# Kernel optimization log

Measured on AMD Instinct MI355X. Metric: run time of the kernel, lower is better.

## Reference

```python
import math
import jax, jax.numpy as jnp
import numpy as np

B, D, C = 2048, 512, 50000
M = math.pi / 6.0
S = 15.0
COS_M, SIN_M = math.cos(M), math.sin(M)
TH = math.cos(math.pi - M)
MM = math.sin(math.pi - M) * M
EPS = 1e-12


def setup_inputs() -> dict:
    key = jax.random.key(0)
    k1, k2, k3 = jax.random.split(key, 3)
    x = jax.random.normal(k1, (B, D), dtype=jnp.float32)
    label = jax.random.randint(k2, (B,), 0, C, dtype=jnp.int64)
    # xavier_normal_ on [C, D]: std = sqrt(2 / (C + D))
    std = math.sqrt(2.0 / (C + D))
    weight = jax.random.normal(k3, (C, D), dtype=jnp.float32) * std
    return {"x": x, "label": label, "weight": weight}


def reference(x, label, weight):
    # L2-normalize rows (F.normalize with eps clamp)
    xn = x / jnp.maximum(jnp.linalg.norm(x, axis=1, keepdims=True), EPS)
    wn = weight / jnp.maximum(jnp.linalg.norm(weight, axis=1, keepdims=True), EPS)
    cosine = xn @ wn.T  # [B, C]

    rows = jnp.arange(cosine.shape[0])
    cos_t = cosine[rows, label]  # target-class cosines [B]
    sin_t = jnp.sqrt(jnp.clip(1.0 - cos_t * cos_t, 0.0, 1.0))
    phi_t = cos_t * COS_M - sin_t * SIN_M
    # easy_margin = False branch
    phi_t = jnp.where(cos_t - TH > 0, phi_t, cos_t - MM)

    # one_hot * phi + (1 - one_hot) * cosine, then scale
    output = S * cosine.at[rows, label].set(phi_t)  # [B, C]

    logp = jax.nn.log_softmax(output, axis=1)
    loss = -jnp.mean(logp[rows, label])
    return output, loss
```

## Files before the change

kernel.cpp:

```cpp
#include <hip/hip_runtime.h>

#define B_ 2048
#define D_ 512
#define C_ 50000
#define NTILEN 391
#define NPART (NTILEN * 2)

static constexpr float S_SCALE = 15.0f;
static constexpr float COS_M_ = 0.86602540378443864676f;
static constexpr float SIN_M_ = 0.5f;
static constexpr float TH_    = -0.86602540378443864676f;
static constexpr float MM_    = 0.26179938779914943654f;

typedef unsigned short u16;
typedef __attribute__((ext_vector_type(4))) float f32x4;
typedef __attribute__((ext_vector_type(8))) short s16x8;

__device__ __forceinline__ u16 f2bf(float f) {
  unsigned u = __float_as_uint(f);
  u += 0x7fffu + ((u >> 16) & 1u);
  return (u16)(u >> 16);
}

__device__ __forceinline__ void load_lds16(const void* g, void* l) {
  __builtin_amdgcn_global_load_lds((const __attribute__((address_space(1))) void*)g,
                                   (__attribute__((address_space(3))) void*)l,
                                   16, 0, 0);
}

__global__ void rownorm_kernel(const float* __restrict__ src, u16* __restrict__ dst,
                               float* __restrict__ loss_zero) {
  const int row = blockIdx.x;
  const int tid = threadIdx.x;
  const float4* s = (const float4*)(src + (size_t)row * D_);
  float4 v = s[tid];
  float ss = v.x * v.x + v.y * v.y + v.z * v.z + v.w * v.w;
#pragma unroll
  for (int mask = 1; mask < 64; mask <<= 1) ss += __shfl_xor(ss, mask);
  __shared__ float red[2];
  if ((tid & 63) == 0) red[tid >> 6] = ss;
  __syncthreads();
  float total = red[0] + red[1];
  float inv = 1.0f / fmaxf(sqrtf(total), 1e-12f);
  ushort4 o;
  o.x = f2bf(v.x * inv); o.y = f2bf(v.y * inv);
  o.z = f2bf(v.z * inv); o.w = f2bf(v.w * inv);
  ((ushort4*)(dst + (size_t)row * D_))[tid] = o;
  if (loss_zero && row == 0 && tid == 0) *loss_zero = 0.0f;
}

__global__ __launch_bounds__(256) void aam_gemm_kernel(
    const u16* __restrict__ xn, const u16* __restrict__ wn,
    const int* __restrict__ label, float* __restrict__ out,
    float* __restrict__ partial, float* __restrict__ target) {
  __shared__ u16 sA[128 * 64];
  __shared__ u16 sB[128 * 64];
  __shared__ int sLbl[128];

  const int tid = threadIdx.x;
  const int m0 = blockIdx.x * 128;
  const int n0 = blockIdx.y * 128;
  const int wave = tid >> 6;
  const int lane = tid & 63;
  const int wm = wave >> 1;
  const int wn_ = wave & 1;

  if (tid < 128) sLbl[tid] = label[m0 + tid];

  f32x4 acc[4][4];
#pragma unroll
  for (int i = 0; i < 4; ++i)
#pragma unroll
    for (int j = 0; j < 4; ++j) {
      f32x4 z = {0.0f, 0.0f, 0.0f, 0.0f};
      acc[i][j] = z;
    }

  for (int kt = 0; kt < D_ / 64; ++kt) {
    const int k0 = kt * 64;
    __syncthreads();
#pragma unroll
    for (int j = 0; j < 4; ++j) {
      const int L = j * 256 + tid;
      const int m = L >> 3;
      const int cs = L & 7;
      const int kc = cs ^ (m & 7);
      load_lds16(xn + (size_t)(m0 + m) * D_ + k0 + kc * 8, &sA[L * 8]);
    }
#pragma unroll
    for (int j = 0; j < 4; ++j) {
      const int L = j * 256 + tid;
      const int m = L >> 3;
      const int cs = L & 7;
      const int kc = cs ^ (m & 7);
      int wr = n0 + m;
      if (wr >= C_) wr = 0;
      load_lds16(wn + (size_t)wr * D_ + k0 + kc * 8, &sB[L * 8]);
    }
    __syncthreads();

#pragma unroll
    for (int kk = 0; kk < 2; ++kk) {
      const int chunk = kk * 4 + (lane >> 4);
      s16x8 af[4], bf[4];
#pragma unroll
      for (int mf = 0; mf < 4; ++mf) {
        const int r = wm * 64 + mf * 16 + (lane & 15);
        const int cs = chunk ^ (r & 7);
        af[mf] = *(const s16x8*)&sA[r * 64 + cs * 8];
      }
#pragma unroll
      for (int nf = 0; nf < 4; ++nf) {
        const int r = wn_ * 64 + nf * 16 + (lane & 15);
        const int cs = chunk ^ (r & 7);
        bf[nf] = *(const s16x8*)&sB[r * 64 + cs * 8];
      }
#pragma unroll
      for (int mf = 0; mf < 4; ++mf)
#pragma unroll
        for (int nf = 0; nf < 4; ++nf)
          acc[mf][nf] = __builtin_amdgcn_mfma_f32_16x16x32_bf16(af[mf], bf[nf],
                                                                acc[mf][nf], 0, 0, 0);
    }
  }

  const int colbase = n0 + wn_ * 64 + (lane & 15);
#pragma unroll
  for (int mf = 0; mf < 4; ++mf) {
#pragma unroll
    for (int reg = 0; reg < 4; ++reg) {
      const int row_l = wm * 64 + mf * 16 + ((lane >> 4) << 2) + reg;
      const int row_g = m0 + row_l;
      const int lbl = sLbl[row_l];
      float v[4];
      float vmax = -INFINITY;
#pragma unroll
      for (int nf = 0; nf < 4; ++nf) {
        const int col = colbase + nf * 16;
        float cv = acc[mf][nf][reg];
        float val = S_SCALE * cv;
        if (col == lbl) {
          float st = sqrtf(fminf(fmaxf(1.0f - cv * cv, 0.0f), 1.0f));
          float phi = cv * COS_M_ - st * SIN_M_;
          float pv = (cv - TH_ > 0.0f) ? phi : (cv - MM_);
          val = S_SCALE * pv;
          target[row_g] = val;
        }
        if (col < C_) {
          out[(size_t)row_g * C_ + col] = val;
          v[nf] = val;
          vmax = fmaxf(vmax, val);
        } else {
          v[nf] = -INFINITY;
        }
      }
#pragma unroll
      for (int mask = 1; mask < 16; mask <<= 1)
        vmax = fmaxf(vmax, __shfl_xor(vmax, mask));
      float sev = 0.0f;
#pragma unroll
      for (int nf = 0; nf < 4; ++nf)
        if (v[nf] != -INFINITY) sev += __expf(v[nf] - vmax);
#pragma unroll
      for (int mask = 1; mask < 16; mask <<= 1) sev += __shfl_xor(sev, mask);
      if ((lane & 15) == 0) {
        float* p = partial + ((size_t)row_g * NPART + (blockIdx.y * 2 + wn_)) * 2;
        p[0] = vmax;
        p[1] = sev;
      }
    }
  }
}

__global__ __launch_bounds__(256) void loss_kernel(const float* __restrict__ partial,
                                                   const float* __restrict__ target,
                                                   float* __restrict__ loss) {
  const int lane = threadIdx.x & 63;
  const int row = blockIdx.x * 4 + (threadIdx.x >> 6);
  float m = -INFINITY, l = 0.0f;
  const float2* p = (const float2*)partial + (size_t)row * NPART;
  for (int i = lane; i < NPART; i += 64) {
    float2 q = p[i];
    if (q.x > m) {
      l = l * __expf(m - q.x) + q.y;
      m = q.x;
    } else if (q.x != -INFINITY) {
      l += q.y * __expf(q.x - m);
    }
  }
#pragma unroll
  for (int mask = 1; mask < 64; mask <<= 1) {
    float m2 = __shfl_xor(m, mask);
    float l2 = __shfl_xor(l, mask);
    if (m2 > m) {
      l = l * __expf(m - m2) + l2;
      m = m2;
    } else if (m2 != -INFINITY) {
      l += l2 * __expf(m2 - m);
    }
  }
  __shared__ float sred[4];
  if (lane == 0) sred[threadIdx.x >> 6] = (m + logf(l)) - target[row];
  __syncthreads();
  if (threadIdx.x == 0)
    atomicAdd(loss, (sred[0] + sred[1] + sred[2] + sred[3]) * (1.0f / 2048.0f));
}

extern "C" void kernel_launch(void* const* d_in, const int* in_sizes, int n_in,
                              void* d_out, int out_size, void* d_ws, size_t ws_size,
                              hipStream_t stream) {
  const float* x = (const float*)d_in[0];
  const int* label = (const int*)d_in[1];
  const float* w = (const float*)d_in[2];
  float* out = (float*)d_out;
  float* loss = out + (size_t)B_ * C_;

  u16* xn = (u16*)d_ws;
  u16* wn = xn + (size_t)B_ * D_;
  float* partial = (float*)(wn + (size_t)C_ * D_);
  float* target = partial + (size_t)B_ * NPART * 2;

  rownorm_kernel<<<B_, 128, 0, stream>>>(x, xn, loss);
  rownorm_kernel<<<C_, 128, 0, stream>>>(w, wn, nullptr);
  aam_gemm_kernel<<<dim3(16, NTILEN), 256, 0, stream>>>(xn, wn, label, out, partial, target);
  loss_kernel<<<B_ / 4, 256, 0, stream>>>(partial, target, loss);
}
```

Before: 725.3 us.

## Double-buffer GEMM LDS loads, remap grid for XCD locality, nontemporal output stores

Splits the GEMM's LDS staging into two buffers so the next K-slice's global-to-LDS loads overlap MFMA work on the current slice, using explicit vmcnt waits and barriers. The grid is flattened and remapped so consecutive blocks on the same XCD share a W tile across the 16 M tiles, aiming to improve L2 reuse of the weight matrix. Output stores become nontemporal to avoid polluting cache with the large logits matrix, and labels are held in registers instead of LDS. Doubling LDS usage may lower occupancy, and the padded grid launches some blocks that exit early.

```diff
diff --git a/kernel.cpp b/kernel.cpp
--- a/kernel.cpp
+++ b/kernel.cpp
@@ -5,6 +5,7 @@
 #define C_ 50000
 #define NTILEN 391
 #define NPART (NTILEN * 2)
+#define PPX 49
 
 static constexpr float S_SCALE = 15.0f;
 static constexpr float COS_M_ = 0.86602540378443864676f;
@@ -53,19 +54,30 @@
     const u16* __restrict__ xn, const u16* __restrict__ wn,
     const int* __restrict__ label, float* __restrict__ out,
     float* __restrict__ partial, float* __restrict__ target) {
-  __shared__ u16 sA[128 * 64];
-  __shared__ u16 sB[128 * 64];
-  __shared__ int sLbl[128];
+  __shared__ u16 sA[2][128 * 64];
+  __shared__ u16 sB[2][128 * 64];
+
+  const int bid = blockIdx.x;
+  const int xcd = bid & 7;
+  const int slot = bid >> 3;
+  const int nt = (slot >> 4) * 8 + xcd;
+  if (nt >= NTILEN) return;
+  const int mt = slot & 15;
+  const int m0 = mt * 128;
+  const int n0 = nt * 128;
 
   const int tid = threadIdx.x;
-  const int m0 = blockIdx.x * 128;
-  const int n0 = blockIdx.y * 128;
   const int wave = tid >> 6;
   const int lane = tid & 63;
   const int wm = wave >> 1;
   const int wn_ = wave & 1;
 
-  if (tid < 128) sLbl[tid] = label[m0 + tid];
+  int lblr[4][4];
+#pragma unroll
+  for (int mf = 0; mf < 4; ++mf)
+#pragma unroll
+    for (int reg = 0; reg < 4; ++reg)
+      lblr[mf][reg] = label[m0 + wm * 64 + mf * 16 + ((lane >> 4) << 2) + reg];
 
   f32x4 acc[4][4];
 #pragma unroll
@@ -76,16 +88,15 @@
       acc[i][j] = z;
     }
 
-  for (int kt = 0; kt < D_ / 64; ++kt) {
+  auto stage = [&](int kt, int b) {
     const int k0 = kt * 64;
-    __syncthreads();
 #pragma unroll
     for (int j = 0; j < 4; ++j) {
       const int L = j * 256 + tid;
       const int m = L >> 3;
       const int cs = L & 7;
       const int kc = cs ^ (m & 7);
-      load_lds16(xn + (size_t)(m0 + m) * D_ + k0 + kc * 8, &sA[L * 8]);
+      load_lds16(xn + (size_t)(m0 + m) * D_ + k0 + kc * 8, &sA[b][L * 8]);
     }
 #pragma unroll
     for (int j = 0; j < 4; ++j) {
@@ -95,10 +106,24 @@
       const int kc = cs ^ (m & 7);
       int wr = n0 + m;
       if (wr >= C_) wr = 0;
-      load_lds16(wn + (size_t)wr * D_ + k0 + kc * 8, &sB[L * 8]);
-    }
-    __syncthreads();
-
+      load_lds16(wn + (size_t)wr * D_ + k0 + kc * 8, &sB[b][L * 8]);
+    }
+  };
+
+  stage(0, 0);
+  int cur = 0;
+  for (int kt = 0; kt < D_ / 64; ++kt) {
+    if (kt + 1 < D_ / 64) {
+      stage(kt + 1, cur ^ 1);
+      asm volatile("s_waitcnt vmcnt(8)" ::: "memory");
+    } else {
+      asm volatile("s_waitcnt vmcnt(0)" ::: "memory");
+    }
+    __builtin_amdgcn_s_barrier();
+    asm volatile("" ::: "memory");
+
+    const u16* __restrict__ A = &sA[cur][0];
+    const u16* __restrict__ Bs = &sB[cur][0];
 #pragma unroll
     for (int kk = 0; kk < 2; ++kk) {
       const int chunk = kk * 4 + (lane >> 4);
@@ -107,13 +132,13 @@
       for (int mf = 0; mf < 4; ++mf) {
         const int r = wm * 64 + mf * 16 + (lane & 15);
         const int cs = chunk ^ (r & 7);
-        af[mf] = *(const s16x8*)&sA[r * 64 + cs * 8];
+        af[mf] = *(const s16x8*)&A[r * 64 + cs * 8];
       }
 #pragma unroll
       for (int nf = 0; nf < 4; ++nf) {
         const int r = wn_ * 64 + nf * 16 + (lane & 15);
         const int cs = chunk ^ (r & 7);
-        bf[nf] = *(const s16x8*)&sB[r * 64 + cs * 8];
+        bf[nf] = *(const s16x8*)&Bs[r * 64 + cs * 8];
       }
 #pragma unroll
       for (int mf = 0; mf < 4; ++mf)
@@ -122,6 +147,10 @@
           acc[mf][nf] = __builtin_amdgcn_mfma_f32_16x16x32_bf16(af[mf], bf[nf],
                                                                 acc[mf][nf], 0, 0, 0);
     }
+    asm volatile("s_waitcnt lgkmcnt(0)" ::: "memory");
+    __builtin_amdgcn_s_barrier();
+    asm volatile("" ::: "memory");
+    cur ^= 1;
   }
 
   const int colbase = n0 + wn_ * 64 + (lane & 15);
@@ -131,7 +160,7 @@
     for (int reg = 0; reg < 4; ++reg) {
       const int row_l = wm * 64 + mf * 16 + ((lane >> 4) << 2) + reg;
       const int row_g = m0 + row_l;
-      const int lbl = sLbl[row_l];
+      const int lbl = lblr[mf][reg];
       float v[4];
       float vmax = -INFINITY;
 #pragma unroll
@@ -147,7 +176,7 @@
           target[row_g] = val;
         }
         if (col < C_) {
-          out[(size_t)row_g * C_ + col] = val;
+          __builtin_nontemporal_store(val, &out[(size_t)row_g * C_ + col]);
           v[nf] = val;
           vmax = fmaxf(vmax, val);
         } else {
@@ -164,7 +193,7 @@
 #pragma unroll
       for (int mask = 1; mask < 16; mask <<= 1) sev += __shfl_xor(sev, mask);
       if ((lane & 15) == 0) {
-        float* p = partial + ((size_t)row_g * NPART + (blockIdx.y * 2 + wn_)) * 2;
+        float* p = partial + ((size_t)row_g * NPART + (nt * 2 + wn_)) * 2;
         p[0] = vmax;
         p[1] = sev;
       }
@@ -222,6 +251,6 @@
 
   rownorm_kernel<<<B_, 128, 0, stream>>>(x, xn, loss);
   rownorm_kernel<<<C_, 128, 0, stream>>>(w, wn, nullptr);
-  aam_gemm_kernel<<<dim3(16, NTILEN), 256, 0, stream>>>(xn, wn, label, out, partial, target);
+  aam_gemm_kernel<<<8 * PPX * 16, 256, 0, stream>>>(xn, wn, label, out, partial, target);
   loss_kernel<<<B_ / 4, 256, 0, stream>>>(partial, target, loss);
 }
```

Result: faster. 645.1 us (-11.1%).
